# Optimization experiments

Measured on AMD Instinct MI355X. Metric: run time of the kernel, lower is better.

The kernel has to match this reference:

```python
import jax, jax.numpy as jnp
import numpy as np

HEADS = 16
D_MODEL = 1024
D_HEAD = D_MODEL // HEADS


def setup_inputs() -> dict:
    key = jax.random.key(0)
    ks = jax.random.split(key, 12)
    B, S = 4, 2048
    scale = D_MODEL ** -0.5
    inp = {
        "q": jax.random.normal(ks[0], (B, S, D_MODEL), jnp.float32),
        "k": jax.random.normal(ks[1], (B, S, D_MODEL), jnp.float32),
        "v": jax.random.normal(ks[2], (B, S, D_MODEL), jnp.float32),
        # causal mask: True = masked position
        "mask": jnp.triu(jnp.ones((S, S), bool), k=1)[None].repeat(B, axis=0),
        "wq": jax.random.normal(ks[3], (D_MODEL, D_MODEL), jnp.float32) * scale,
        "bq": jnp.zeros((D_MODEL,), jnp.float32),
        "wk": jax.random.normal(ks[4], (D_MODEL, D_MODEL), jnp.float32) * scale,
        "bk": jnp.zeros((D_MODEL,), jnp.float32),
        "wv": jax.random.normal(ks[5], (D_MODEL, D_MODEL), jnp.float32) * scale,
        "bv": jnp.zeros((D_MODEL,), jnp.float32),
        "wo": jax.random.normal(ks[6], (D_MODEL, D_MODEL), jnp.float32) * scale,
        "bo": jnp.zeros((D_MODEL,), jnp.float32),
    }
    return inp


def _split_head(x):
    B, S, _ = x.shape
    return x.reshape(B, S, HEADS, D_HEAD).transpose(0, 2, 1, 3)  # [B,H,S,D]


def reference(q, k, v, mask, wq, bq, wk, bk, wv, bv, wo, bo):
    # linear projections (torch Linear: x @ W^T + b)
    qh = _split_head(q @ wq.T + bq) * (D_HEAD ** -0.5)
    kh = _split_head(k @ wk.T + bk)
    vh = _split_head(v @ wv.T + bv)
    # scores [B,H,Sq,Sk]
    scores = jnp.einsum("bhqd,bhkd->bhqk", qh, kh)
    scores = jnp.where(mask[:, None, :, :], -1e20, scores)
    weights = jax.nn.softmax(scores, axis=-1)  # dropout p=0 in eval
    ctx = jnp.einsum("bhqk,bhkd->bhqd", weights, vh)
    B, H, S, D = ctx.shape
    ctx = ctx.transpose(0, 2, 1, 3).reshape(B, S, H * D)
    return ctx @ wo.T + bo
```

## Files before the change

kernel.cpp:

```cpp
#include <hip/hip_runtime.h>
#include <hip/hip_bf16.h>
#include <cstdint>
#include <cstddef>

typedef unsigned short u16;
typedef unsigned int u32;
using short8  = __attribute__((ext_vector_type(8))) short;
using f32x4   = __attribute__((ext_vector_type(4))) float;
using f32x16  = __attribute__((ext_vector_type(16))) float;
using u32x4   = __attribute__((ext_vector_type(4))) u32;

#define SCALE_Q 0.18033688011112043f

#define WAITVM(N) asm volatile("s_waitcnt vmcnt(" #N ")" ::: "memory")
#define LGKM0    asm volatile("s_waitcnt lgkmcnt(0)" ::: "memory")
#define BARX     __builtin_amdgcn_s_barrier()
#define SCHED0   __builtin_amdgcn_sched_barrier(0)

__device__ inline u16 f2bf(float f) {
  return __builtin_bit_cast(u16, __float2bfloat16(f));
}

__device__ inline u32 cvt_pk_bf16(float a, float b) {
  u32 r;
  asm("v_cvt_pk_bf16_f32 %0, %1, %2" : "=v"(r) : "v"(a), "v"(b));
  return r;
}

__device__ inline f32x4 mfma16(short8 a, short8 b, f32x4 c) {
  return __builtin_amdgcn_mfma_f32_16x16x32_bf16(a, b, c, 0, 0, 0);
}
__device__ inline f32x16 mfma32(short8 a, short8 b, f32x16 c) {
  return __builtin_amdgcn_mfma_f32_32x32x16_bf16(a, b, c, 0, 0, 0);
}

__device__ inline void gload16(const void* g, void* l) {
  __builtin_amdgcn_global_load_lds(
      (const __attribute__((address_space(1))) void*)g,
      (__attribute__((address_space(3))) void*)l,
      16, 0, 0);
}

__global__ __launch_bounds__(256)
void prep(const float* __restrict__ wq, const float* __restrict__ wk,
          const float* __restrict__ wv, const float* __restrict__ wo,
          u16* __restrict__ Wb) {
  const int c = blockIdx.x * 256 + threadIdx.x;
  const int m = c >> 17;
  const size_t off = (size_t)(c & 131071) * 8;
  const float* src = (m == 0) ? wq : (m == 1) ? wk : (m == 2) ? wv : wo;
  const float sc = (m == 0) ? SCALE_Q : 1.f;
  f32x4 a = *(const f32x4*)(src + off);
  f32x4 b = *(const f32x4*)(src + off + 4);
  short8 vv;
#pragma unroll
  for (int j = 0; j < 4; ++j) { vv[j] = (short)f2bf(a[j] * sc); vv[4 + j] = (short)f2bf(b[j] * sc); }
  *(short8*)&Wb[(size_t)m * 1048576 + off] = vv;
}

struct GemmArgs {
  const float* qf; const float* kf; const float* vf;
  const u16* ctx; const u16* Wb;
  const float* bq; const float* bk; const float* bv; const float* bo;
  u16* Qs; u16* Ks; u16* Vs; float* out;
};

template<bool FUSED>
__global__ __launch_bounds__(256, 2)
void gemm_proj(GemmArgs ga, int modeBase) {
  const int mode = modeBase + blockIdx.z;
  const int bx = blockIdx.x;
  const int bm = ((bx & 7) << 3) | (bx >> 3);
  const int bn = blockIdx.y;
  const int tid = threadIdx.x;
  const int w = tid >> 6, lane = tid & 63;
  const int wr = w >> 1, wc = w & 1;
  const int l15 = lane & 15, g = lane >> 4;

  const float* Af = (mode == 0) ? ga.qf : (mode == 1) ? ga.kf : ga.vf;
  const u16*   Am = ga.ctx;
  const u16*   Wm = ga.Wb + (size_t)mode * 1048576;
  const float* bias = (mode == 0) ? ga.bq : (mode == 1) ? ga.bk : (mode == 2) ? ga.bv : ga.bo;

  __shared__ u16 As[2][128 * 64];
  __shared__ u16 Bs[3][128 * 64];

  f32x4 acc[4][4] = {};
  const int m0 = bm * 128, n0 = bn * 128;

  const int r_lo = lane >> 3;
  const int sc8 = ((lane & 7) ^ (lane >> 3)) * 8;

  auto stageB = [&](int k0, int slot) {
#pragma unroll
    for (int i = 0; i < 4; ++i)
      gload16(Wm + (size_t)(n0 + i * 32 + w * 8 + r_lo) * 1024 + k0 + sc8,
              &Bs[slot][i * 2048 + w * 512]);
  };
  auto stageA_lds = [&](int k0, int slot) {
#pragma unroll
    for (int i = 0; i < 4; ++i)
      gload16(Am + (size_t)(m0 + i * 32 + w * 8 + r_lo) * 1024 + k0 + sc8,
              &As[slot][i * 2048 + w * 512]);
  };
  auto loadA = [&](int k0, f32x4 (&r)[8]) {
#pragma unroll
    for (int i = 0; i < 4; ++i) {
      const float* src = Af + (size_t)(m0 + i * 32 + w * 8 + r_lo) * 1024 + k0 + sc8;
      r[2 * i]     = *(const f32x4*)(src);
      r[2 * i + 1] = *(const f32x4*)(src + 4);
    }
  };
  auto writeA = [&](f32x4 (&r)[8], int slot) {
#pragma unroll
    for (int i = 0; i < 4; ++i) {
      u32x4 wv;
      wv[0] = cvt_pk_bf16(r[2 * i][0], r[2 * i][1]);
      wv[1] = cvt_pk_bf16(r[2 * i][2], r[2 * i][3]);
      wv[2] = cvt_pk_bf16(r[2 * i + 1][0], r[2 * i + 1][1]);
      wv[3] = cvt_pk_bf16(r[2 * i + 1][2], r[2 * i + 1][3]);
      *(u32x4*)&As[slot][i * 2048 + w * 512 + lane * 8] = wv;
    }
  };

  auto compute = [&](int aslot, int bslot) {
#pragma unroll
    for (int kk = 0; kk < 2; ++kk) {
      short8 av[4], bv4[4];
#pragma unroll
      for (int mi = 0; mi < 4; ++mi) {
        const int row = wr * 64 + mi * 16 + l15;
        av[mi] = *(const short8*)&As[aslot][row * 64 + ((((kk << 2) | g)) ^ (row & 7)) * 8];
      }
#pragma unroll
      for (int ni = 0; ni < 4; ++ni) {
        const int row = wc * 64 + ni * 16 + l15;
        bv4[ni] = *(const short8*)&Bs[bslot][row * 64 + ((((kk << 2) | g)) ^ (row & 7)) * 8];
      }
#pragma unroll
      for (int mi = 0; mi < 4; ++mi)
#pragma unroll
        for (int ni = 0; ni < 4; ++ni)
          acc[mi][ni] = mfma16(av[mi], bv4[ni], acc[mi][ni]);
    }
  };

  if (FUSED) {
    f32x4 rA[8], rB[8];
    stageB(0, 0); stageB(64, 1);
    loadA(0, rA); loadA(64, rB);
    WAITVM(8);
    writeA(rA, 0);
    LGKM0;

    int bs0 = 0;
    for (int p = 0; p < 14; p += 2) {
      int bs1 = bs0 + 1; if (bs1 == 3) bs1 = 0;
      int bs2 = bs1 + 1; if (bs2 == 3) bs2 = 0;
      BARX; SCHED0;
      stageB((p + 2) * 64, bs2);
      compute(0, bs0);
      WAITVM(4);
      writeA(rB, 1);
      loadA((p + 2) * 64, rA);
      LGKM0;
      BARX; SCHED0;
      stageB((p + 3) * 64, bs0);
      compute(1, bs1);
      WAITVM(4);
      writeA(rA, 0);
      loadA((p + 3) * 64, rB);
      LGKM0;
      bs0 = bs2;
    }
    BARX; SCHED0;
    compute(0, bs0);
    WAITVM(0);
    writeA(rB, 1);
    LGKM0;
    BARX; SCHED0;
    compute(1, (bs0 + 1 == 3) ? 0 : bs0 + 1);
  } else {
    stageA_lds(0, 0);  stageB(0, 0);
    stageA_lds(64, 1); stageB(64, 1);
#pragma unroll 2
    for (int t = 0; t < 14; ++t) {
      WAITVM(8);
      BARX; SCHED0;
      compute(t & 1, t & 1);
      BARX; SCHED0;
      stageA_lds((t + 2) * 64, t & 1); stageB((t + 2) * 64, t & 1);
    }
    WAITVM(8);
    BARX; SCHED0;
    compute(0, 0);
    WAITVM(0);
    BARX; SCHED0;
    compute(1, 1);
  }

  float bvals[4];
#pragma unroll
  for (int ni = 0; ni < 4; ++ni)
    bvals[ni] = bias[n0 + wc * 64 + ni * 16 + l15] * ((mode == 0) ? SCALE_Q : 1.f);

  if (mode == 3) {
#pragma unroll
    for (int mi = 0; mi < 4; ++mi)
#pragma unroll
      for (int ni = 0; ni < 4; ++ni)
#pragma unroll
        for (int r = 0; r < 4; ++r) {
          const int m = m0 + wr * 64 + mi * 16 + g * 4 + r;
          const int n = n0 + wc * 64 + ni * 16 + l15;
          ga.out[(size_t)m * 1024 + n] = acc[mi][ni][r] + bvals[ni];
        }
  } else {
    u16* O = (mode == 0) ? ga.Qs : (mode == 1) ? ga.Ks : ga.Vs;
#pragma unroll
    for (int mi = 0; mi < 4; ++mi)
#pragma unroll
      for (int ni = 0; ni < 4; ++ni)
#pragma unroll
        for (int r = 0; r < 4; ++r) {
          const int m = m0 + wr * 64 + mi * 16 + g * 4 + r;
          const int n = n0 + wc * 64 + ni * 16 + l15;
          const int b = m >> 11, s = m & 2047, hh = n >> 6, d = n & 63;
          const float val = acc[mi][ni][r] + bvals[ni];
          const size_t base = (size_t)(b * 16 + hh) * 131072;
          size_t idx;
          if (mode == 2) {
            const int sp = (s & ~12) | ((s & 4) << 1) | ((s & 8) >> 1);
            const int kt = sp >> 5, w5 = sp & 31;
            const int j = ((d >> 5) << 1) | (w5 >> 4);
            const int hi2 = (w5 >> 3) & 1, e = w5 & 7;
            idx = base + (size_t)kt * 2048 + j * 512 + hi2 * 256 + (d & 31) * 8 + e;
          } else {
            const int s32 = s >> 5, l31 = s & 31;
            const int t2 = d >> 4, hi2 = (d >> 3) & 1, e = d & 7;
            idx = base + (size_t)s32 * 2048 + t2 * 512 + hi2 * 256 + l31 * 8 + e;
          }
          O[idx] = f2bf(val);
        }
  }
}

__global__ __launch_bounds__(256)
void attn_fwd(const u16* __restrict__ Qs, const u16* __restrict__ Ks,
              const u16* __restrict__ Vs, u16* __restrict__ ctx) {
  const int bh = blockIdx.x;
  const int qt = 15 - blockIdx.y;
  const int tid = threadIdx.x;
  const int w = tid >> 6, lane = tid & 63;
  const int l31 = lane & 31, hi = lane >> 5;

  const u16* Qb = Qs + (size_t)bh * 131072;
  const u16* Kb = Ks + (size_t)bh * 131072;
  const u16* Vb = Vs + (size_t)bh * 131072;
  const int b = bh >> 4, hh = bh & 15;

  const int qw0 = qt * 128 + w * 32;
  const int nktw = (qw0 >> 5) + 1;
  const int npair = qt * 2 + 2;
  const int qrow = qw0 + l31;

  __shared__ u16 Klds[2][2][2048];
  __shared__ u16 Vlds[2][2][2048];

  auto stagePair = [&](int pr, int slot) {
    const size_t t0 = (size_t)(2 * pr) * 2048 + (w * 64 + lane) * 8;
    gload16(Kb + t0,        &Klds[slot][0][w * 512]);
    gload16(Kb + t0 + 2048, &Klds[slot][1][w * 512]);
    gload16(Vb + t0,        &Vlds[slot][0][w * 512]);
    gload16(Vb + t0 + 2048, &Vlds[slot][1][w * 512]);
  };

  stagePair(0, 0);
  stagePair(1, 1);
  SCHED0;

  short8 qf[4];
  {
    const u16* qp = Qb + (size_t)(qw0 >> 5) * 2048 + lane * 8;
#pragma unroll
    for (int t = 0; t < 4; ++t) qf[t] = *(const short8*)(qp + t * 512);
  }
  SCHED0;

  f32x16 oacc0 = {}, oacc1 = {};
  float lsum = 0.f;

  for (int pr = 0; pr < npair; ++pr) {
    const int slot = pr & 1;
    if (pr + 1 < npair) { WAITVM(4); } else { WAITVM(0); }
    BARX; SCHED0;

#pragma unroll
    for (int j = 0; j < 2; ++j) {
      const int kt = 2 * pr + j;

      short8 kf[4], vf[4];
#pragma unroll
      for (int t = 0; t < 4; ++t) {
        kf[t] = *(const short8*)&Klds[slot][j][t * 512 + lane * 8];
        vf[t] = *(const short8*)&Vlds[slot][j][t * 512 + lane * 8];
      }

      f32x16 st = {};
      __builtin_amdgcn_s_setprio(1);
      st = mfma32(kf[0], qf[0], st);
      st = mfma32(kf[1], qf[1], st);
      st = mfma32(kf[2], qf[2], st);
      st = mfma32(kf[3], qf[3], st);
      __builtin_amdgcn_s_setprio(0);

      if (kt >= nktw - 1) {
#pragma unroll
        for (int r = 0; r < 16; ++r) {
          const int ka = kt * 32 + (r & 3) + 8 * (r >> 2) + 4 * hi;
          if (ka > qrow) st[r] = -1e30f;
        }
      }

      float p[16];
#pragma unroll
      for (int r = 0; r < 16; ++r) p[r] = __builtin_amdgcn_exp2f(st[r]);
      {
        float s0 = (p[0] + p[1]) + (p[2] + p[3]);
        float s1 = (p[4] + p[5]) + (p[6] + p[7]);
        float s2 = (p[8] + p[9]) + (p[10] + p[11]);
        float s3 = (p[12] + p[13]) + (p[14] + p[15]);
        lsum += (s0 + s1) + (s2 + s3);
      }
      u32x4 a0, a1;
#pragma unroll
      for (int v2 = 0; v2 < 4; ++v2) {
        a0[v2] = cvt_pk_bf16(p[2 * v2], p[2 * v2 + 1]);
        a1[v2] = cvt_pk_bf16(p[8 + 2 * v2], p[9 + 2 * v2]);
      }
      const short8 pb0 = __builtin_bit_cast(short8, a0);
      const short8 pb1 = __builtin_bit_cast(short8, a1);
      __builtin_amdgcn_s_setprio(1);
      oacc0 = mfma32(vf[0], pb0, oacc0);
      oacc0 = mfma32(vf[1], pb1, oacc0);
      oacc1 = mfma32(vf[2], pb0, oacc1);
      oacc1 = mfma32(vf[3], pb1, oacc1);
      __builtin_amdgcn_s_setprio(0);
    }

    BARX; SCHED0;
    if (pr + 2 < npair) stagePair(pr + 2, slot);
  }

  lsum += __shfl_xor(lsum, 32);
  const float inv = __builtin_amdgcn_rcpf(lsum);

  u16* crow = ctx + ((size_t)(b * 2048 + qrow)) * 1024 + hh * 64;
#pragma unroll
  for (int r = 0; r < 16; r += 2) {
    const int d0 = (r & 3) + 8 * (r >> 2) + 4 * hi;
    *(u32*)&crow[d0]      = cvt_pk_bf16(oacc0[r] * inv, oacc0[r + 1] * inv);
    *(u32*)&crow[32 + d0] = cvt_pk_bf16(oacc1[r] * inv, oacc1[r + 1] * inv);
  }
}

extern "C" void kernel_launch(void* const* d_in, const int* in_sizes, int n_in,
                              void* d_out, int out_size, void* d_ws, size_t ws_size,
                              hipStream_t stream) {
  const float* q  = (const float*)d_in[0];
  const float* k  = (const float*)d_in[1];
  const float* v  = (const float*)d_in[2];
  const float* wq = (const float*)d_in[4];
  const float* bq = (const float*)d_in[5];
  const float* wk = (const float*)d_in[6];
  const float* bk = (const float*)d_in[7];
  const float* wv = (const float*)d_in[8];
  const float* bv = (const float*)d_in[9];
  const float* wo = (const float*)d_in[10];
  const float* bo = (const float*)d_in[11];

  char* ws = (char*)d_ws;
  const size_t WBSZ = (size_t)4 * 1048576 * sizeof(u16);
  const size_t SZ   = (size_t)64 * 131072 * sizeof(u16);
  u16* Wb  = (u16*)(ws);
  u16* Qs  = (u16*)(ws + WBSZ);
  u16* Ks  = (u16*)(ws + WBSZ + SZ);
  u16* Vs  = (u16*)(ws + WBSZ + 2 * SZ);
  u16* ctx = (u16*)(ws + WBSZ + 3 * SZ);

  GemmArgs ga;
  ga.qf = q; ga.kf = k; ga.vf = v; ga.ctx = ctx; ga.Wb = Wb;
  ga.bq = bq; ga.bk = bk; ga.bv = bv; ga.bo = bo;
  ga.Qs = Qs; ga.Ks = Ks; ga.Vs = Vs; ga.out = (float*)d_out;

  prep<<<dim3(2048), dim3(256), 0, stream>>>(wq, wk, wv, wo, Wb);
  gemm_proj<true><<<dim3(64, 8, 3), dim3(256), 0, stream>>>(ga, 0);
  attn_fwd<<<dim3(64, 16), dim3(256), 0, stream>>>(Qs, Ks, Vs, ctx);
  gemm_proj<false><<<dim3(64, 8, 1), dim3(256), 0, stream>>>(ga, 3);
}
```

Before: 163.4 us.

## Pre-swizzle weights into MFMA fragment order and load B directly to registers

The weight-prep kernel now writes the bf16 weights in a per-tile, per-wave fragment layout. The projection GEMMs can then load B operands straight from global memory into registers, with no LDS staging and no LDS reads. This drops the triple-buffered B LDS array and its ds_read traffic, and the lower LDS use may allow more occupancy. In exchange it adds 16 VGPRs of B fragments per buffer and relies on global/L2 latency being hidden. The fused path now waits on vmcnt(0) each half-step, which may expose load latency.

```diff
diff --git a/kernel.cpp b/kernel.cpp
--- a/kernel.cpp
+++ b/kernel.cpp
@@ -44,23 +44,29 @@
 __global__ __launch_bounds__(256)
 void prep(const float* __restrict__ wq, const float* __restrict__ wk,
           const float* __restrict__ wv, const float* __restrict__ wo,
-          u16* __restrict__ Wb) {
+          u16* __restrict__ Wf) {
   const int c = blockIdx.x * 256 + threadIdx.x;
   const int m = c >> 17;
-  const size_t off = (size_t)(c & 131071) * 8;
+  const int off = (c & 131071) * 8;
+  const int n = off >> 10, k0 = off & 1023;
   const float* src = (m == 0) ? wq : (m == 1) ? wk : (m == 2) ? wv : wo;
   const float sc = (m == 0) ? SCALE_Q : 1.f;
-  f32x4 a = *(const f32x4*)(src + off);
-  f32x4 b = *(const f32x4*)(src + off + 4);
+  f32x4 a = *(const f32x4*)(src + (size_t)n * 1024 + k0);
+  f32x4 b = *(const f32x4*)(src + (size_t)n * 1024 + k0 + 4);
   short8 vv;
 #pragma unroll
   for (int j = 0; j < 4; ++j) { vv[j] = (short)f2bf(a[j] * sc); vv[4 + j] = (short)f2bf(b[j] * sc); }
-  *(short8*)&Wb[(size_t)m * 1048576 + off] = vv;
+  const int bn = n >> 7, r = n & 127;
+  const int wc = r >> 6, ni = (r >> 4) & 3, l15 = r & 15;
+  const int kt = k0 >> 6, kk = (k0 >> 5) & 1, g = (k0 >> 3) & 3;
+  const size_t dst = (size_t)m * 1048576 + (size_t)bn * 131072 + (size_t)kt * 8192
+                   + wc * 4096 + (ni * 2 + kk) * 512 + (l15 * 4 + g) * 8;
+  *(short8*)&Wf[dst] = vv;
 }
 
 struct GemmArgs {
   const float* qf; const float* kf; const float* vf;
-  const u16* ctx; const u16* Wb;
+  const u16* ctx; const u16* Wf;
   const float* bq; const float* bk; const float* bv; const float* bo;
   u16* Qs; u16* Ks; u16* Vs; float* out;
 };
@@ -79,11 +85,10 @@
 
   const float* Af = (mode == 0) ? ga.qf : (mode == 1) ? ga.kf : ga.vf;
   const u16*   Am = ga.ctx;
-  const u16*   Wm = ga.Wb + (size_t)mode * 1048576;
+  const u16*   WfM = ga.Wf + (size_t)mode * 1048576;
   const float* bias = (mode == 0) ? ga.bq : (mode == 1) ? ga.bk : (mode == 2) ? ga.bv : ga.bo;
 
   __shared__ u16 As[2][128 * 64];
-  __shared__ u16 Bs[3][128 * 64];
 
   f32x4 acc[4][4] = {};
   const int m0 = bm * 128, n0 = bn * 128;
@@ -91,11 +96,12 @@
   const int r_lo = lane >> 3;
   const int sc8 = ((lane & 7) ^ (lane >> 3)) * 8;
 
-  auto stageB = [&](int k0, int slot) {
-#pragma unroll
-    for (int i = 0; i < 4; ++i)
-      gload16(Wm + (size_t)(n0 + i * 32 + w * 8 + r_lo) * 1024 + k0 + sc8,
-              &Bs[slot][i * 2048 + w * 512]);
+  const u16* WfB = WfM + (size_t)bn * 131072 + wc * 4096 + (l15 * 4 + g) * 8;
+
+  auto loadB = [&](int kt, short8 (&b)[8]) {
+    const u16* p = WfB + (size_t)kt * 8192;
+#pragma unroll
+    for (int f = 0; f < 8; ++f) b[f] = *(const short8*)(p + f * 512);
   };
   auto stageA_lds = [&](int k0, int slot) {
 #pragma unroll
@@ -123,80 +129,71 @@
     }
   };
 
-  auto compute = [&](int aslot, int bslot) {
+  auto compute = [&](int aslot, short8 (&b)[8]) {
 #pragma unroll
     for (int kk = 0; kk < 2; ++kk) {
-      short8 av[4], bv4[4];
+      short8 av[4];
 #pragma unroll
       for (int mi = 0; mi < 4; ++mi) {
         const int row = wr * 64 + mi * 16 + l15;
         av[mi] = *(const short8*)&As[aslot][row * 64 + ((((kk << 2) | g)) ^ (row & 7)) * 8];
       }
 #pragma unroll
-      for (int ni = 0; ni < 4; ++ni) {
-        const int row = wc * 64 + ni * 16 + l15;
-        bv4[ni] = *(const short8*)&Bs[bslot][row * 64 + ((((kk << 2) | g)) ^ (row & 7)) * 8];
-      }
-#pragma unroll
       for (int mi = 0; mi < 4; ++mi)
 #pragma unroll
         for (int ni = 0; ni < 4; ++ni)
-          acc[mi][ni] = mfma16(av[mi], bv4[ni], acc[mi][ni]);
+          acc[mi][ni] = mfma16(av[mi], b[ni * 2 + kk], acc[mi][ni]);
     }
   };
 
   if (FUSED) {
     f32x4 rA[8], rB[8];
-    stageB(0, 0); stageB(64, 1);
-    loadA(0, rA); loadA(64, rB);
-    WAITVM(8);
+    short8 bA[8], bB[8];
+    loadB(0, bA); loadA(0, rA);
+    loadB(1, bB); loadA(64, rB);
+    WAITVM(16);
     writeA(rA, 0);
     LGKM0;
 
-    int bs0 = 0;
     for (int p = 0; p < 14; p += 2) {
-      int bs1 = bs0 + 1; if (bs1 == 3) bs1 = 0;
-      int bs2 = bs1 + 1; if (bs2 == 3) bs2 = 0;
       BARX; SCHED0;
-      stageB((p + 2) * 64, bs2);
-      compute(0, bs0);
-      WAITVM(4);
+      compute(0, bA);
+      WAITVM(0);
       writeA(rB, 1);
-      loadA((p + 2) * 64, rA);
+      loadB(p + 2, bA); loadA((p + 2) * 64, rA);
       LGKM0;
       BARX; SCHED0;
-      stageB((p + 3) * 64, bs0);
-      compute(1, bs1);
-      WAITVM(4);
+      compute(1, bB);
+      WAITVM(0);
       writeA(rA, 0);
-      loadA((p + 3) * 64, rB);
+      loadB(p + 3, bB); loadA((p + 3) * 64, rB);
       LGKM0;
-      bs0 = bs2;
-    }
-    BARX; SCHED0;
-    compute(0, bs0);
+    }
+    BARX; SCHED0;
+    compute(0, bA);
     WAITVM(0);
     writeA(rB, 1);
     LGKM0;
     BARX; SCHED0;
-    compute(1, (bs0 + 1 == 3) ? 0 : bs0 + 1);
+    compute(1, bB);
   } else {
-    stageA_lds(0, 0);  stageB(0, 0);
-    stageA_lds(64, 1); stageB(64, 1);
-#pragma unroll 2
+    short8 bA[8], bB[8];
+    stageA_lds(0, 0);  loadB(0, bA);
+    stageA_lds(64, 1); loadB(1, bB);
     for (int t = 0; t < 14; ++t) {
-      WAITVM(8);
+      WAITVM(12);
       BARX; SCHED0;
-      compute(t & 1, t & 1);
+      if (t & 1) compute(1, bB); else compute(0, bA);
       BARX; SCHED0;
-      stageA_lds((t + 2) * 64, t & 1); stageB((t + 2) * 64, t & 1);
-    }
-    WAITVM(8);
-    BARX; SCHED0;
-    compute(0, 0);
+      stageA_lds((t + 2) * 64, t & 1);
+      if (t & 1) loadB(t + 2, bB); else loadB(t + 2, bA);
+    }
+    WAITVM(12);
+    BARX; SCHED0;
+    compute(0, bA);
     WAITVM(0);
     BARX; SCHED0;
-    compute(1, 1);
+    compute(1, bB);
   }
 
   float bvals[4];
@@ -382,18 +379,18 @@
   char* ws = (char*)d_ws;
   const size_t WBSZ = (size_t)4 * 1048576 * sizeof(u16);
   const size_t SZ   = (size_t)64 * 131072 * sizeof(u16);
-  u16* Wb  = (u16*)(ws);
+  u16* Wf  = (u16*)(ws);
   u16* Qs  = (u16*)(ws + WBSZ);
   u16* Ks  = (u16*)(ws + WBSZ + SZ);
   u16* Vs  = (u16*)(ws + WBSZ + 2 * SZ);
   u16* ctx = (u16*)(ws + WBSZ + 3 * SZ);
 
   GemmArgs ga;
-  ga.qf = q; ga.kf = k; ga.vf = v; ga.ctx = ctx; ga.Wb = Wb;
+  ga.qf = q; ga.kf = k; ga.vf = v; ga.ctx = ctx; ga.Wf = Wf;
   ga.bq = bq; ga.bk = bk; ga.bv = bv; ga.bo = bo;
   ga.Qs = Qs; ga.Ks = Ks; ga.Vs = Vs; ga.out = (float*)d_out;
 
-  prep<<<dim3(2048), dim3(256), 0, stream>>>(wq, wk, wv, wo, Wb);
+  prep<<<dim3(2048), dim3(256), 0, stream>>>(wq, wk, wv, wo, Wf);
   gemm_proj<true><<<dim3(64, 8, 3), dim3(256), 0, stream>>>(ga, 0);
   attn_fwd<<<dim3(64, 16), dim3(256), 0, stream>>>(Qs, Ks, Vs, ctx);
   gemm_proj<false><<<dim3(64, 8, 1), dim3(256), 0, stream>>>(ga, 3);
```

Measured after the change: 183.4 us. 12.3% more time.
